# Kernel tuning notes

Hardware: AMD Instinct MI355X
Metric: run time of the kernel (lower is better)

The kernel has to match this reference:

```python
import jax, jax.numpy as jnp
import numpy as np

B, S, D = 4, 2048, 1024
NH, NKV = 16, 4
DK = D // NH          # 64
NG = NH // NKV        # 4


def _rope_tables(seq, d_k):
    theta = 1.0 / jnp.power(10000.0, jnp.arange(0, d_k, 2, dtype=jnp.float32) / d_k)
    ang = jnp.outer(jnp.arange(seq, dtype=jnp.float32), theta)  # [S, DK/2]
    ang = jnp.concatenate([ang, ang], axis=-1)                   # [S, DK]
    return jnp.cos(ang), jnp.sin(ang)


def _rotate_half(t):
    half = t.shape[-1] // 2
    return jnp.concatenate([-t[..., half:], t[..., :half]], axis=-1)


def _apply_rope(t, cos, sin):
    # t: [B, H, S, DK]; cos/sin: [S, DK]
    return t * cos + _rotate_half(t) * sin


def setup_inputs() -> dict:
    key = jax.random.key(0)
    ks = jax.random.split(key, 5)
    sc = 0.02
    x = jax.random.normal(ks[0], (B, S, D), dtype=jnp.float32)
    Wq = jax.random.normal(ks[1], (D, NH * DK), dtype=jnp.float32) * sc
    Wk = jax.random.normal(ks[2], (D, NKV * DK), dtype=jnp.float32) * sc
    Wv = jax.random.normal(ks[3], (D, NKV * DK), dtype=jnp.float32) * sc
    Wo = jax.random.normal(ks[4], (D, D), dtype=jnp.float32) * sc
    mask = jnp.tril(jnp.ones((S, S), dtype=bool))[None, None]  # causal [1,1,S,S]
    return {"x": x, "Wq": Wq, "Wk": Wk, "Wv": Wv, "Wo": Wo, "mask": mask}


def reference(x, Wq, Wk, Wv, Wo, mask):
    batch, seq, _ = x.shape
    q = (x @ Wq).reshape(batch, seq, NH, DK).transpose(0, 2, 1, 3)    # [B,NH,S,DK]
    k = (x @ Wk).reshape(batch, seq, NKV, DK).transpose(0, 2, 1, 3)   # [B,NKV,S,DK]
    v = (x @ Wv).reshape(batch, seq, NKV, DK).transpose(0, 2, 1, 3)

    cos, sin = _rope_tables(seq, DK)
    q = _apply_rope(q, cos, sin)
    k = _apply_rope(k, cos, sin)

    # GQA: repeat_interleave K/V along head dim
    k = jnp.repeat(k, NG, axis=1)  # [B,NH,S,DK]
    v = jnp.repeat(v, NG, axis=1)

    scores = jnp.einsum('bhqd,bhkd->bhqk', q, k) / jnp.sqrt(jnp.float32(DK))
    scores = jnp.where(mask, scores, jnp.float32(-jnp.inf))
    weights = jax.nn.softmax(scores, axis=-1)
    out = jnp.einsum('bhqk,bhkd->bhqd', weights, v)          # [B,NH,S,DK]
    out = out.transpose(0, 2, 1, 3).reshape(batch, seq, D)   # [B,S,D]
    return out @ Wo
```

## Files before the change

### kernel.cpp

```cpp
#include <hip/hip_runtime.h>

#define DEV __device__ __forceinline__

typedef short s16x8 __attribute__((ext_vector_type(8)));
typedef float f32x4 __attribute__((ext_vector_type(4)));


DEV unsigned short f2bf(float f) {
  union { float f; unsigned int u; } a; a.f = f;
  unsigned int u = a.u;
  u = (u + 0x7FFFu + ((u >> 16) & 1u)) >> 16;
  return (unsigned short)u;
}

DEV unsigned int bfpack2(float a, float b) {
  union { float f; unsigned int u; } x, y; x.f = a; y.f = b;
  return ((x.u + 0x8000u) >> 16) | ((y.u + 0x8000u) & 0xFFFF0000u);
}

DEV unsigned int pktrunc(float a, float b) {
  union { float f; unsigned int u; } x, y; x.f = a; y.f = b;
  return __builtin_amdgcn_perm(y.u, x.u, 0x07060302u);
}

DEV void gl_lds16(const void* g, void* l) {
  __builtin_amdgcn_global_load_lds(
      (const __attribute__((address_space(1))) unsigned int*)g,
      (__attribute__((address_space(3))) unsigned int*)l, 16, 0, 0);
}

__global__ __launch_bounds__(256) void cvt_kern(const float* __restrict__ src,
                                                unsigned short* __restrict__ dst) {
  int i = blockIdx.x * 256 + threadIdx.x;
  float4 v = ((const float4*)src)[i];
  ushort4 o = make_ushort4(f2bf(v.x), f2bf(v.y), f2bf(v.z), f2bf(v.w));
  ((ushort4*)dst)[i] = o;
}

__global__ __launch_bounds__(256) void transp_all(const float* __restrict__ Wq,
                                                  const float* __restrict__ Wk,
                                                  const float* __restrict__ Wv,
                                                  const float* __restrict__ Wo,
                                                  unsigned short* __restrict__ WqkvT,
                                                  unsigned short* __restrict__ WoT) {
  __shared__ float tile[32][33];
  int k0 = blockIdx.x * 32, n0 = blockIdx.y * 32;
  const float* src; int sc, nloc, drow;
  unsigned short* dst;
  if (n0 < 1024)      { src = Wq; sc = 1024; nloc = n0;        dst = WqkvT; drow = n0; }
  else if (n0 < 1280) { src = Wk; sc = 256;  nloc = n0 - 1024; dst = WqkvT; drow = n0; }
  else if (n0 < 1536) { src = Wv; sc = 256;  nloc = n0 - 1280; dst = WqkvT; drow = n0; }
  else                { src = Wo; sc = 1024; nloc = n0 - 1536; dst = WoT;   drow = n0 - 1536; }
  int tx = threadIdx.x & 31, ty = threadIdx.x >> 5;
  #pragma unroll
  for (int i = ty; i < 32; i += 8)
    tile[i][tx] = src[(k0 + i) * sc + (nloc + tx)];
  __syncthreads();
  #pragma unroll
  for (int i = ty; i < 32; i += 8)
    dst[(size_t)(drow + i) * 1024 + (k0 + tx)] = f2bf(tile[tx][i]);
}

template <int EPI>
__global__ __launch_bounds__(256, 4) void gemm128(
    const unsigned short* __restrict__ A,
    const unsigned short* __restrict__ BT,
    unsigned short* __restrict__ Qbuf,
    unsigned short* __restrict__ Kbuf,
    unsigned short* __restrict__ VTbuf,
    float* __restrict__ Cout) {
  __shared__ __align__(16) unsigned short As[2][128 * 32];
  __shared__ __align__(16) unsigned short Bs[2][128 * 32];
  const int K = 1024;
  const int NKT = K / 32;
  int m0 = blockIdx.x * 128, n0 = blockIdx.y * 128;
  int tid = threadIdx.x, w = tid >> 6, lane = tid & 63;
  int c4 = lane & 15, quad = lane >> 4;
  int x3 = c4 & 3;
  int m_off = (w & 1) * 64, n_off = (w >> 1) * 64;

  f32x4 acc[4][4];
  #pragma unroll
  for (int i = 0; i < 4; i++)
    #pragma unroll
    for (int j = 0; j < 4; j++) acc[i][j] = (f32x4){0.f, 0.f, 0.f, 0.f};

  const unsigned short* pA[2];
  const unsigned short* pB[2];
  #pragma unroll
  for (int i = 0; i < 2; ++i) {
    int slot = i * 256 + tid;
    int row = slot >> 2, cs = slot & 3, lc = cs ^ (row & 3);
    pA[i] = A + (size_t)(m0 + row) * K + lc * 8;
    pB[i] = BT + (size_t)(n0 + row) * K + lc * 8;
  }

  #pragma unroll
  for (int i = 0; i < 2; ++i) {
    int slot = i * 256 + tid;
    gl_lds16(pA[i], (char*)As[0] + slot * 16);
    gl_lds16(pB[i], (char*)Bs[0] + slot * 16);
    pA[i] += 32; pB[i] += 32;
  }

  int cc = (quad ^ x3) * 16;
  for (int kt = 0; kt < NKT; ++kt) {
    int cur = kt & 1, nxt = cur ^ 1;
    __syncthreads();

    if (kt + 1 < NKT) {
      #pragma unroll
      for (int i = 0; i < 2; ++i) {
        int slot = i * 256 + tid;
        gl_lds16(pA[i], (char*)As[nxt] + slot * 16);
        gl_lds16(pB[i], (char*)Bs[nxt] + slot * 16);
        pA[i] += 32; pB[i] += 32;
      }
    }

    s16x8 a[4], b[4];
    #pragma unroll
    for (int mi = 0; mi < 4; ++mi)
      a[mi] = *(const s16x8*)((const char*)As[cur] + (m_off + mi * 16 + c4) * 64 + cc);
    #pragma unroll
    for (int ni = 0; ni < 4; ++ni)
      b[ni] = *(const s16x8*)((const char*)Bs[cur] + (n_off + ni * 16 + c4) * 64 + cc);
    #pragma unroll
    for (int mi = 0; mi < 4; ++mi)
      #pragma unroll
      for (int ni = 0; ni < 4; ++ni)
        acc[mi][ni] = __builtin_amdgcn_mfma_f32_16x16x32_bf16(a[mi], b[ni], acc[mi][ni], 0, 0, 0);
  }

  if (EPI == 1) {
    #pragma unroll
    for (int mi = 0; mi < 4; ++mi)
      #pragma unroll
      for (int ni = 0; ni < 4; ++ni)
        #pragma unroll
        for (int r = 0; r < 4; ++r) {
          int row = m0 + m_off + mi * 16 + quad * 4 + r;
          int col = n0 + n_off + ni * 16 + c4;
          Cout[(size_t)row * 1024 + col] = acc[mi][ni][r];
        }
  } else {
    int colbase = n0 + n_off;
    if (colbase < 1280) {
      const float CTH = 0.41524101186092029f;
      const float SC = 0.18033688011112042f;
      float th0 = exp2f(-(float)c4 * CTH);
      float th1 = exp2f(-(float)(c4 + 16) * CTH);
      bool isQ = colbase < 1024;
      float osc = isQ ? SC : 1.0f;
      #pragma unroll
      for (int mi = 0; mi < 4; ++mi)
        #pragma unroll
        for (int r = 0; r < 4; ++r) {
          int row = m0 + m_off + mi * 16 + quad * 4 + r;
          float pos = (float)(row & 2047);
          float a0 = pos * th0, a1 = pos * th1;
          float c0 = __cosf(a0), s0 = __sinf(a0);
          float c1 = __cosf(a1), s1 = __sinf(a1);
          float v0 = acc[mi][0][r], v1 = acc[mi][1][r];
          float v2 = acc[mi][2][r], v3 = acc[mi][3][r];
          float o0 = (v0 * c0 - v2 * s0) * osc;
          float o1 = (v1 * c1 - v3 * s1) * osc;
          float o2 = (v2 * c0 + v0 * s0) * osc;
          float o3 = (v3 * c1 + v1 * s1) * osc;
          if (isQ) {
            size_t base = (size_t)row * 1024 + colbase + c4;
            Qbuf[base] = f2bf(o0); Qbuf[base + 16] = f2bf(o1);
            Qbuf[base + 32] = f2bf(o2); Qbuf[base + 48] = f2bf(o3);
          } else {
            size_t base = (size_t)row * 256 + (colbase - 1024) + c4;
            Kbuf[base] = f2bf(o0); Kbuf[base + 16] = f2bf(o1);
            Kbuf[base + 32] = f2bf(o2); Kbuf[base + 48] = f2bf(o3);
          }
        }
    } else {
      #pragma unroll
      for (int mi = 0; mi < 4; ++mi)
        #pragma unroll
        for (int ni = 0; ni < 4; ++ni) {
          int row = m0 + m_off + mi * 16 + quad * 4;
          int c = colbase + ni * 16 + c4 - 1280;
          int bb = row >> 11, s = row & 2047;
          uint2 pv = make_uint2(bfpack2(acc[mi][ni][0], acc[mi][ni][1]),
                                bfpack2(acc[mi][ni][2], acc[mi][ni][3]));
          *(uint2*)(VTbuf + ((size_t)(bb * 256 + c)) * 2048 + s) = pv;
        }
    }
  }
}

__global__ __launch_bounds__(128, 2) void attn_kern(
    const unsigned short* __restrict__ Qbuf,
    const unsigned short* __restrict__ Kbuf,
    const unsigned short* __restrict__ VTbuf,
    unsigned short* __restrict__ Obuf) {
  __shared__ __align__(16) unsigned short Ks[2][64 * 64];
  __shared__ __align__(16) unsigned short VTs[2][64 * 64];
  __shared__ __align__(16) unsigned short Ps[2 * 32 * 64];

  int pr = blockIdx.x;
  int h = blockIdx.y, b = blockIdx.z, g = h >> 2;
  int tid = threadIdx.x, w = tid >> 6, lane = tid & 63;
  int c4 = lane & 15, quad = lane >> 4;
  int x7 = c4 & 7;
  unsigned short* Pw = Ps + w * 2048;

  const unsigned short* kB[4];
  const unsigned short* vB[4];
  #pragma unroll
  for (int i = 0; i < 4; ++i) {
    int L = i * 128 + tid;
    int row = L >> 3, cs = (L & 7) ^ (row & 7);
    kB[i] = Kbuf + (size_t)(b * 2048 + row) * 256 + g * 64 + cs * 8;
    vB[i] = VTbuf + (size_t)(b * 256 + g * 64 + row) * 2048 + cs * 8;
  }

  for (int ph = 0; ph < 2; ++ph) {
    int qtile = ph ? (31 - pr) : pr;
    int nkv = qtile + 1;
    int q0 = qtile * 64;

    s16x8 bq[2][2];
    #pragma unroll
    for (int gg = 0; gg < 2; ++gg)
      #pragma unroll
      for (int kk = 0; kk < 2; ++kk)
        bq[gg][kk] = *(const s16x8*)(Qbuf +
            (size_t)(b * 2048 + q0 + w * 32 + gg * 16 + c4) * 1024 +
            h * 64 + kk * 32 + quad * 8);

    const unsigned short* kS[4];
    const unsigned short* vS[4];
    #pragma unroll
    for (int i = 0; i < 4; ++i) { kS[i] = kB[i]; vS[i] = vB[i]; }

    f32x4 Oacc[2][4];
    float lacc[2] = {0.f, 0.f};
    #pragma unroll
    for (int gg = 0; gg < 2; ++gg)
      #pragma unroll
      for (int nd = 0; nd < 4; ++nd) Oacc[gg][nd] = (f32x4){0.f, 0.f, 0.f, 0.f};

    __syncthreads();
    #pragma unroll
    for (int i = 0; i < 4; ++i) {
      int L = i * 128 + tid;
      gl_lds16(kS[i], (char*)Ks[0] + L * 16);
      gl_lds16(vS[i], (char*)VTs[0] + L * 16);
      kS[i] += 64 * 256; vS[i] += 64;
    }

    for (int kt = 0; kt < nkv; ++kt) {
      int cur = kt & 1, nxt = cur ^ 1;
      __syncthreads();

      if (kt + 1 < nkv) {
        #pragma unroll
        for (int i = 0; i < 4; ++i) {
          int L = i * 128 + tid;
          gl_lds16(kS[i], (char*)Ks[nxt] + L * 16);
          gl_lds16(vS[i], (char*)VTs[nxt] + L * 16);
          kS[i] += 64 * 256; vS[i] += 64;
        }
      }

      const char* Kc = (const char*)Ks[cur];
      const char* Vc = (const char*)VTs[cur];

      f32x4 st[2][4];
      #pragma unroll
      for (int gg = 0; gg < 2; ++gg)
        #pragma unroll
        for (int mt = 0; mt < 4; ++mt) st[gg][mt] = (f32x4){0.f, 0.f, 0.f, 0.f};
      #pragma unroll
      for (int kk = 0; kk < 2; ++kk) {
        #pragma unroll
        for (int mt = 0; mt < 4; ++mt) {
          s16x8 ak = *(const s16x8*)(Kc + (mt * 16 + c4) * 128 +
                                     ((kk * 4 + quad) ^ x7) * 16);
          st[0][mt] = __builtin_amdgcn_mfma_f32_16x16x32_bf16(ak, bq[0][kk], st[0][mt], 0, 0, 0);
          st[1][mt] = __builtin_amdgcn_mfma_f32_16x16x32_bf16(ak, bq[1][kk], st[1][mt], 0, 0, 0);
        }
      }

      #pragma unroll
      for (int gg = 0; gg < 2; ++gg) {
        int qmin = q0 + w * 32 + gg * 16;
        if (kt * 64 + 63 > qmin) {
          int qi = qmin + c4;
          #pragma unroll
          for (int mt = 0; mt < 4; ++mt)
            #pragma unroll
            for (int r = 0; r < 4; ++r) {
              int kv = kt * 64 + mt * 16 + quad * 4 + r;
              if (kv > qi) st[gg][mt][r] = -1e30f;
            }
        }
        int rr = gg * 16 + c4;
        #pragma unroll
        for (int mt = 0; mt < 4; ++mt) {
          float e0 = exp2f(st[gg][mt][0]);
          float e1 = exp2f(st[gg][mt][1]);
          float e2 = exp2f(st[gg][mt][2]);
          float e3 = exp2f(st[gg][mt][3]);
          lacc[gg] += (e0 + e1) + (e2 + e3);
          unsigned int lo = pktrunc(e0, e1);
          unsigned int hi = pktrunc(e2, e3);
          int cc = (mt * 2 + (quad >> 1)) ^ x7;
          *(uint2*)((char*)Pw + rr * 128 + cc * 16 + (quad & 1) * 8) =
              make_uint2(lo, hi);
        }
      }

      #pragma unroll
      for (int kk = 0; kk < 2; ++kk) {
        s16x8 ap0 = *(const s16x8*)((const char*)Pw + c4 * 128 +
                                    ((kk * 4 + quad) ^ x7) * 16);
        s16x8 ap1 = *(const s16x8*)((const char*)Pw + (16 + c4) * 128 +
                                    ((kk * 4 + quad) ^ x7) * 16);
        #pragma unroll
        for (int nd = 0; nd < 4; ++nd) {
          s16x8 av = *(const s16x8*)(Vc + (nd * 16 + c4) * 128 +
                                     ((kk * 4 + quad) ^ x7) * 16);
          Oacc[0][nd] = __builtin_amdgcn_mfma_f32_16x16x32_bf16(av, ap0, Oacc[0][nd], 0, 0, 0);
          Oacc[1][nd] = __builtin_amdgcn_mfma_f32_16x16x32_bf16(av, ap1, Oacc[1][nd], 0, 0, 0);
        }
      }
    }

    #pragma unroll
    for (int gg = 0; gg < 2; ++gg) {
      float ls = lacc[gg];
      ls += __shfl_xor(ls, 16);
      ls += __shfl_xor(ls, 32);
      float linv = 1.f / ls;
      int rr = gg * 16 + c4;
      #pragma unroll
      for (int nd = 0; nd < 4; ++nd) {
        unsigned int lo = bfpack2(Oacc[gg][nd][0] * linv, Oacc[gg][nd][1] * linv);
        unsigned int hi = bfpack2(Oacc[gg][nd][2] * linv, Oacc[gg][nd][3] * linv);
        int cc = (nd * 2 + (quad >> 1)) ^ x7;
        *(uint2*)((char*)Pw + rr * 128 + cc * 16 + (quad & 1) * 8) =
            make_uint2(lo, hi);
      }
    }
    {
      int row = lane >> 1;
      int grow = b * 2048 + q0 + w * 32 + row;
      #pragma unroll
      for (int j = 0; j < 4; ++j) {
        int cb = (lane & 1) * 4 + j;
        uint4 v = *(const uint4*)((const char*)Pw + row * 128 +
                                  (cb ^ (row & 7)) * 16);
        *(uint4*)(Obuf + (size_t)grow * 1024 + h * 64 + cb * 8) = v;
      }
    }
  }
}

extern "C" void kernel_launch(void* const* d_in, const int* in_sizes, int n_in,
                              void* d_out, int out_size, void* d_ws, size_t ws_size,
                              hipStream_t stream) {
  const float* x  = (const float*)d_in[0];
  const float* Wq = (const float*)d_in[1];
  const float* Wk = (const float*)d_in[2];
  const float* Wv = (const float*)d_in[3];
  const float* Wo = (const float*)d_in[4];
  float* out = (float*)d_out;

  unsigned short* xb    = (unsigned short*)d_ws;
  unsigned short* WqkvT = xb + 8192 * 1024;
  unsigned short* WoT   = WqkvT + 1536 * 1024;
  unsigned short* Qbuf  = WoT + 1024 * 1024;
  unsigned short* Kbuf  = Qbuf + 8192 * 1024;
  unsigned short* VTbuf = Kbuf + 8192 * 256;
  unsigned short* Obuf  = VTbuf + 4 * 256 * 2048;

  cvt_kern<<<8192, 256, 0, stream>>>(x, xb);
  transp_all<<<dim3(32, 80), 256, 0, stream>>>(Wq, Wk, Wv, Wo, WqkvT, WoT);

  gemm128<0><<<dim3(64, 12), 256, 0, stream>>>(xb, WqkvT, Qbuf, Kbuf, VTbuf, nullptr);
  attn_kern<<<dim3(16, 16, 4), 128, 0, stream>>>(Qbuf, Kbuf, VTbuf, Obuf);
  gemm128<1><<<dim3(64, 8), 256, 0, stream>>>(Obuf, WoT, nullptr, nullptr, nullptr, out);
}
```

Measured before the change: 239.6 us.

## Share K/V tiles across two GQA heads per attention block; merge prep kernels

The attention kernel now runs 4 waves per block, covering two query heads of the same KV group, so each K/V tile loaded into LDS serves two heads instead of one. This halves the K/V global traffic and the grid size, at the cost of larger LDS use for P staging and a higher thread count per block. The bf16 conversion of x and the weight transposes are also fused into one launch to save a kernel launch.

New measurement: 232.7 us. -2.9%, faster.

```diff
diff --git a/kernel.cpp b/kernel.cpp
--- a/kernel.cpp
+++ b/kernel.cpp
@@ -29,22 +29,25 @@
       (__attribute__((address_space(3))) unsigned int*)l, 16, 0, 0);
 }
 
-__global__ __launch_bounds__(256) void cvt_kern(const float* __restrict__ src,
-                                                unsigned short* __restrict__ dst) {
-  int i = blockIdx.x * 256 + threadIdx.x;
-  float4 v = ((const float4*)src)[i];
-  ushort4 o = make_ushort4(f2bf(v.x), f2bf(v.y), f2bf(v.z), f2bf(v.w));
-  ((ushort4*)dst)[i] = o;
-}
-
-__global__ __launch_bounds__(256) void transp_all(const float* __restrict__ Wq,
-                                                  const float* __restrict__ Wk,
-                                                  const float* __restrict__ Wv,
-                                                  const float* __restrict__ Wo,
-                                                  unsigned short* __restrict__ WqkvT,
-                                                  unsigned short* __restrict__ WoT) {
+__global__ __launch_bounds__(256) void prep_kern(const float* __restrict__ x,
+                                                 const float* __restrict__ Wq,
+                                                 const float* __restrict__ Wk,
+                                                 const float* __restrict__ Wv,
+                                                 const float* __restrict__ Wo,
+                                                 unsigned short* __restrict__ xb,
+                                                 unsigned short* __restrict__ WqkvT,
+                                                 unsigned short* __restrict__ WoT) {
+  int bid = blockIdx.x;
+  if (bid < 8192) {
+    int i = bid * 256 + threadIdx.x;
+    float4 v = ((const float4*)x)[i];
+    ushort4 o = make_ushort4(f2bf(v.x), f2bf(v.y), f2bf(v.z), f2bf(v.w));
+    ((ushort4*)xb)[i] = o;
+    return;
+  }
+  int tb = bid - 8192;
+  int k0 = (tb & 31) * 32, n0 = (tb >> 5) * 32;
   __shared__ float tile[32][33];
-  int k0 = blockIdx.x * 32, n0 = blockIdx.y * 32;
   const float* src; int sc, nloc, drow;
   unsigned short* dst;
   if (n0 < 1024)      { src = Wq; sc = 1024; nloc = n0;        dst = WqkvT; drow = n0; }
@@ -193,27 +196,31 @@
   }
 }
 
-__global__ __launch_bounds__(128, 2) void attn_kern(
+__global__ __launch_bounds__(256, 3) void attn_kern(
     const unsigned short* __restrict__ Qbuf,
     const unsigned short* __restrict__ Kbuf,
     const unsigned short* __restrict__ VTbuf,
     unsigned short* __restrict__ Obuf) {
   __shared__ __align__(16) unsigned short Ks[2][64 * 64];
   __shared__ __align__(16) unsigned short VTs[2][64 * 64];
-  __shared__ __align__(16) unsigned short Ps[2 * 32 * 64];
+  __shared__ __align__(16) unsigned short Ps[4 * 32 * 64];
 
   int pr = blockIdx.x;
-  int h = blockIdx.y, b = blockIdx.z, g = h >> 2;
+  int g = blockIdx.y >> 1;
+  int hp = blockIdx.y & 1;
+  int b = blockIdx.z;
   int tid = threadIdx.x, w = tid >> 6, lane = tid & 63;
+  int h = g * 4 + hp * 2 + (w >> 1);
+  int qh = w & 1;
   int c4 = lane & 15, quad = lane >> 4;
   int x7 = c4 & 7;
   unsigned short* Pw = Ps + w * 2048;
 
-  const unsigned short* kB[4];
-  const unsigned short* vB[4];
-  #pragma unroll
-  for (int i = 0; i < 4; ++i) {
-    int L = i * 128 + tid;
+  const unsigned short* kB[2];
+  const unsigned short* vB[2];
+  #pragma unroll
+  for (int i = 0; i < 2; ++i) {
+    int L = i * 256 + tid;
     int row = L >> 3, cs = (L & 7) ^ (row & 7);
     kB[i] = Kbuf + (size_t)(b * 2048 + row) * 256 + g * 64 + cs * 8;
     vB[i] = VTbuf + (size_t)(b * 256 + g * 64 + row) * 2048 + cs * 8;
@@ -230,13 +237,13 @@
       #pragma unroll
       for (int kk = 0; kk < 2; ++kk)
         bq[gg][kk] = *(const s16x8*)(Qbuf +
-            (size_t)(b * 2048 + q0 + w * 32 + gg * 16 + c4) * 1024 +
+            (size_t)(b * 2048 + q0 + qh * 32 + gg * 16 + c4) * 1024 +
             h * 64 + kk * 32 + quad * 8);
 
-    const unsigned short* kS[4];
-    const unsigned short* vS[4];
-    #pragma unroll
-    for (int i = 0; i < 4; ++i) { kS[i] = kB[i]; vS[i] = vB[i]; }
+    const unsigned short* kS[2];
+    const unsigned short* vS[2];
+    #pragma unroll
+    for (int i = 0; i < 2; ++i) { kS[i] = kB[i]; vS[i] = vB[i]; }
 
     f32x4 Oacc[2][4];
     float lacc[2] = {0.f, 0.f};
@@ -247,8 +254,8 @@
 
     __syncthreads();
     #pragma unroll
-    for (int i = 0; i < 4; ++i) {
-      int L = i * 128 + tid;
+    for (int i = 0; i < 2; ++i) {
+      int L = i * 256 + tid;
       gl_lds16(kS[i], (char*)Ks[0] + L * 16);
       gl_lds16(vS[i], (char*)VTs[0] + L * 16);
       kS[i] += 64 * 256; vS[i] += 64;
@@ -260,8 +267,8 @@
 
       if (kt + 1 < nkv) {
         #pragma unroll
-        for (int i = 0; i < 4; ++i) {
-          int L = i * 128 + tid;
+        for (int i = 0; i < 2; ++i) {
+          int L = i * 256 + tid;
           gl_lds16(kS[i], (char*)Ks[nxt] + L * 16);
           gl_lds16(vS[i], (char*)VTs[nxt] + L * 16);
           kS[i] += 64 * 256; vS[i] += 64;
@@ -289,7 +296,7 @@
 
       #pragma unroll
       for (int gg = 0; gg < 2; ++gg) {
-        int qmin = q0 + w * 32 + gg * 16;
+        int qmin = q0 + qh * 32 + gg * 16;
         if (kt * 64 + 63 > qmin) {
           int qi = qmin + c4;
           #pragma unroll
@@ -350,7 +357,7 @@
     }
     {
       int row = lane >> 1;
-      int grow = b * 2048 + q0 + w * 32 + row;
+      int grow = b * 2048 + q0 + qh * 32 + row;
       #pragma unroll
       for (int j = 0; j < 4; ++j) {
         int cb = (lane & 1) * 4 + j;
@@ -380,10 +387,9 @@
   unsigned short* VTbuf = Kbuf + 8192 * 256;
   unsigned short* Obuf  = VTbuf + 4 * 256 * 2048;
 
-  cvt_kern<<<8192, 256, 0, stream>>>(x, xb);
-  transp_all<<<dim3(32, 80), 256, 0, stream>>>(Wq, Wk, Wv, Wo, WqkvT, WoT);
+  prep_kern<<<8192 + 2560, 256, 0, stream>>>(x, Wq, Wk, Wv, Wo, xb, WqkvT, WoT);
 
   gemm128<0><<<dim3(64, 12), 256, 0, stream>>>(xb, WqkvT, Qbuf, Kbuf, VTbuf, nullptr);
-  attn_kern<<<dim3(16, 16, 4), 128, 0, stream>>>(Qbuf, Kbuf, VTbuf, Obuf);
+  attn_kern<<<dim3(16, 8, 4), 256, 0, stream>>>(Qbuf, Kbuf, VTbuf, Obuf);
   gemm128<1><<<dim3(64, 8), 256, 0, stream>>>(Obuf, WoT, nullptr, nullptr, nullptr, out);
 }
```
